# Kernel optimization log

Measured on AMD Instinct MI355X. Metric: run time of the kernel, lower is better.

The kernel has to match this reference:

```python
import jax, jax.numpy as jnp
import numpy as np

HIDDEN = 4096
HEADS = 32
HEAD_DIM = HIDDEN // HEADS  # 128; kv length must equal this (additive-bias broadcast)
B, SQ, SK = 4, 2048, HEAD_DIM


def _split_heads(x):
    # [B, T, HIDDEN] -> [B, H, T, d]
    b, t, _ = x.shape
    return x.reshape(b, t, HEADS, HEAD_DIM).transpose(0, 2, 1, 3)


def setup_inputs() -> dict:
    key = jax.random.key(0)
    ks = jax.random.split(key, 8)
    s = 1.0 / np.sqrt(HIDDEN)
    return {
        "q": jax.random.normal(ks[0], (B, SQ, HIDDEN), jnp.float32),
        "k": jax.random.normal(ks[1], (B, SK, HIDDEN), jnp.float32),
        "v": jax.random.normal(ks[2], (B, SK, HIDDEN), jnp.float32),
        "r": jax.random.normal(ks[3], (B, SQ, HIDDEN), jnp.float32),
        "Wq": jax.random.normal(ks[4], (HIDDEN, HIDDEN), jnp.float32) * s,
        "Wk": jax.random.normal(ks[5], (HIDDEN, HIDDEN), jnp.float32) * s,
        "Wv": jax.random.normal(ks[6], (HIDDEN, HIDDEN), jnp.float32) * s,
        "Wo": jax.random.normal(ks[7], (HIDDEN, HIDDEN), jnp.float32) * s,
    }


def reference(q, k, v, r, Wq, Wk, Wv, Wo):
    qh = _split_heads(q @ Wq)           # [B,H,SQ,d]
    kh = _split_heads(k @ Wk)           # [B,H,SK,d]
    vh = _split_heads(v @ Wv)           # [B,H,SK,d]
    rh = _split_heads(r @ Wo)           # [B,H,SQ,d] ; d == SK, added as bias
    scale = 1.0 / np.sqrt(HEAD_DIM).astype(np.float32)
    scores = jnp.einsum("bhqd,bhkd->bhqk", qh, kh) * scale + rh
    attn = jax.nn.softmax(scores, axis=-1)
    ctx = jnp.einsum("bhqk,bhkd->bhqd", attn, vh)       # [B,H,SQ,d]
    ctx = ctx.transpose(0, 2, 1, 3).reshape(q.shape[0], -1, HIDDEN)
    return ctx @ Wo  # Wo reused for output projection, as in source
```

## Files before the change

kernel.cpp:

```cpp
#include <hip/hip_runtime.h>
#include <hip/hip_bf16.h>

typedef unsigned short u16;
typedef unsigned int   u32;
typedef unsigned long long u64;
typedef __attribute__((ext_vector_type(8))) short short8;
typedef __attribute__((ext_vector_type(4))) float f32x4;

#define HID   4096
#define NHEAD 32
#define HD    128
#define NB    4
#define NSQ   2048
#define NSK   128
#define MROWS (NB*NSQ)
#define KROWS (NB*NSK)

__device__ __forceinline__ u16 f2bf(float f) {
  u32 u = __builtin_bit_cast(u32, f);
  u += 0x7fffu + ((u >> 16) & 1u);
  return (u16)(u >> 16);
}

__device__ __forceinline__ u64 pack4(float4 f) {
  return (u64)f2bf(f.x) | ((u64)f2bf(f.y) << 16) |
         ((u64)f2bf(f.z) << 32) | ((u64)f2bf(f.w) << 48);
}

__device__ __forceinline__ uint4 packu16x8(const u16* v) {
  uint4 o;
  o.x = (u32)v[0] | ((u32)v[1] << 16);
  o.y = (u32)v[2] | ((u32)v[3] << 16);
  o.z = (u32)v[4] | ((u32)v[5] << 16);
  o.w = (u32)v[6] | ((u32)v[7] << 16);
  return o;
}

__device__ __forceinline__ f32x4 mfma16(short8 a, short8 b, f32x4 c) {
  return __builtin_amdgcn_mfma_f32_16x16x32_bf16(a, b, c, 0, 0, 0);
}

__device__ __forceinline__ void gload_lds16(const u16* g, u16* l) {
  __builtin_amdgcn_global_load_lds((const __attribute__((address_space(1))) u32*)g,
                                   (__attribute__((address_space(3))) u32*)l, 16, 0, 0);
}

__global__ __launch_bounds__(256) void convert_bf16(const float* __restrict__ in,
                                                    u16* __restrict__ out, long long n4)
{
  long long i = (long long)blockIdx.x * blockDim.x + threadIdx.x;
  const long long stride = (long long)gridDim.x * blockDim.x;
  for (; i < n4; i += stride) {
    float4 f = ((const float4*)in)[i];
    ((u64*)out)[i] = pack4(f);
  }
}

__global__ __launch_bounds__(256) void transpose_convert(const float* __restrict__ W,
                                                         u16* __restrict__ Wt)
{
  __shared__ __align__(16) u16 tile[64][72];
  const int t = threadIdx.x;
  const int c0 = blockIdx.x * 64, r0 = blockIdx.y * 64;
  #pragma unroll
  for (int i = 0; i < 4; ++i) {
    int e = i * 1024 + t * 4;
    int rr = e >> 6, cc = e & 63;
    float4 f = *(const float4*)(W + (size_t)(r0 + rr) * HID + c0 + cc);
    *(u64*)&tile[rr][cc] = pack4(f);
  }
  __syncthreads();
  #pragma unroll
  for (int i = 0; i < 2; ++i) {
    int e = i * 2048 + t * 8;
    int cc = e >> 6, rr = e & 63;
    u16 vals[8];
    #pragma unroll
    for (int jj = 0; jj < 8; ++jj) vals[jj] = tile[rr + jj][cc];
    *(uint4*)(Wt + (size_t)(c0 + cc) * HID + r0 + rr) = packu16x8(vals);
  }
}

__global__ __launch_bounds__(256) void transpose_head(const u16* __restrict__ Vh,
                                                      u16* __restrict__ VT)
{
  __shared__ __align__(16) u16 tile[128][136];
  const int t = threadIdx.x;
  const int bh = blockIdx.x;
  const int b = bh >> 5, h = bh & 31;
  #pragma unroll
  for (int i = 0; i < 8; ++i) {
    int e = i * 2048 + t * 8;
    int tr = e >> 7, d = e & 127;
    *(uint4*)&tile[tr][d] = *(const uint4*)(Vh + ((size_t)b * NSK + tr) * HID + h * HD + d);
  }
  __syncthreads();
  #pragma unroll
  for (int i = 0; i < 8; ++i) {
    int e = i * 2048 + t * 8;
    int d = e >> 7, tt = e & 127;
    u16 vals[8];
    #pragma unroll
    for (int jj = 0; jj < 8; ++jj) vals[jj] = tile[tt + jj][d];
    *(uint4*)(VT + ((size_t)bh * HD + d) * NSK + tt) = packu16x8(vals);
  }
}


__device__ __forceinline__ short8 ldf(const u16* buf, int r, int cb) {
  return *(const short8*)(buf + r * 64 + (cb ^ ((r & 7) << 3)));
}

__device__ __forceinline__ void stage2(u16* dst, const u16* g, long off0, long off1, int tid) {
  gload_lds16(g + off0, dst + tid * 8);
  gload_lds16(g + off1, dst + 4096 + tid * 8);
}

template<bool S1, bool S2, int VM>
__device__ __forceinline__ void tile8(const u16* __restrict__ Ag, const u16* __restrict__ Bg,
                                      int kt, u16* Ac, u16* Bc, u16* Ao, u16* Bo,
                                      int wm, int wn, int g, int c16,
                                      long off0, long off1, int tid, f32x4 (&acc)[8][4])
{
  const int g8 = g * 8;
  short8 af[4][2], bf[4][2];

  #pragma unroll
  for (int i = 0; i < 4; ++i) {
    const int r = wm * 128 + i * 16 + c16;
    af[i][0] = ldf(Ac, r, g8); af[i][1] = ldf(Ac, r, 32 + g8);
  }
  #pragma unroll
  for (int j = 0; j < 2; ++j) {
    const int r = wn * 64 + j * 16 + c16;
    bf[j][0] = ldf(Bc, r, g8); bf[j][1] = ldf(Bc, r, 32 + g8);
  }
  if constexpr (S1) stage2(Ao + 8192, Ag + (size_t)128 * HID + kt + 64, off0, off1, tid);
  __builtin_amdgcn_s_barrier();
  asm volatile("s_waitcnt lgkmcnt(0)" ::: "memory");
  __builtin_amdgcn_sched_barrier(0);
  __builtin_amdgcn_s_setprio(1);
  #pragma unroll
  for (int i = 0; i < 4; ++i)
    #pragma unroll
    for (int j = 0; j < 2; ++j) {
      acc[i][j] = mfma16(af[i][0], bf[j][0], acc[i][j]);
      acc[i][j] = mfma16(af[i][1], bf[j][1], acc[i][j]);
    }
  __builtin_amdgcn_s_setprio(0);
  __builtin_amdgcn_s_barrier();

  #pragma unroll
  for (int j = 2; j < 4; ++j) {
    const int r = wn * 64 + j * 16 + c16;
    bf[j][0] = ldf(Bc, r, g8); bf[j][1] = ldf(Bc, r, 32 + g8);
  }
  if constexpr (S1) stage2(Bo + 8192, Bg + (size_t)128 * HID + kt + 64, off0, off1, tid);
  __builtin_amdgcn_s_barrier();
  asm volatile("s_waitcnt lgkmcnt(0)" ::: "memory");
  __builtin_amdgcn_sched_barrier(0);
  __builtin_amdgcn_s_setprio(1);
  #pragma unroll
  for (int i = 0; i < 4; ++i)
    #pragma unroll
    for (int j = 2; j < 4; ++j) {
      acc[i][j] = mfma16(af[i][0], bf[j][0], acc[i][j]);
      acc[i][j] = mfma16(af[i][1], bf[j][1], acc[i][j]);
    }
  __builtin_amdgcn_s_setprio(0);
  __builtin_amdgcn_s_barrier();

  #pragma unroll
  for (int i = 0; i < 4; ++i) {
    const int r = wm * 128 + 64 + i * 16 + c16;
    af[i][0] = ldf(Ac, r, g8); af[i][1] = ldf(Ac, r, 32 + g8);
  }
  if constexpr (S2) stage2(Bc, Bg + kt + 128, off0, off1, tid);
  __builtin_amdgcn_s_barrier();
  asm volatile("s_waitcnt lgkmcnt(0)" ::: "memory");
  __builtin_amdgcn_sched_barrier(0);
  __builtin_amdgcn_s_setprio(1);
  #pragma unroll
  for (int i = 0; i < 4; ++i)
    #pragma unroll
    for (int j = 0; j < 2; ++j) {
      acc[4 + i][j] = mfma16(af[i][0], bf[j][0], acc[4 + i][j]);
      acc[4 + i][j] = mfma16(af[i][1], bf[j][1], acc[4 + i][j]);
    }
  __builtin_amdgcn_s_setprio(0);
  __builtin_amdgcn_s_barrier();

  if constexpr (S2) stage2(Ac, Ag + kt + 128, off0, off1, tid);
  __builtin_amdgcn_s_barrier();
  __builtin_amdgcn_s_setprio(1);
  #pragma unroll
  for (int i = 0; i < 4; ++i)
    #pragma unroll
    for (int j = 2; j < 4; ++j) {
      acc[4 + i][j] = mfma16(af[i][0], bf[j][0], acc[4 + i][j]);
      acc[4 + i][j] = mfma16(af[i][1], bf[j][1], acc[4 + i][j]);
    }
  __builtin_amdgcn_s_setprio(0);
  if constexpr (VM == 4) {
    asm volatile("s_waitcnt vmcnt(4)" ::: "memory");
    __builtin_amdgcn_sched_barrier(0);
  } else if constexpr (VM == 0) {
    asm volatile("s_waitcnt vmcnt(0)" ::: "memory");
    __builtin_amdgcn_sched_barrier(0);
  }
  __builtin_amdgcn_s_barrier();
}

template<bool OUTF32>
__global__ __launch_bounds__(512, 2) void gemm256(const u16* __restrict__ A,
                                                  const u16* __restrict__ Bt,
                                                  void* __restrict__ Cv)
{
  __shared__ __align__(16) u16 As[2][16384];
  __shared__ __align__(16) u16 Bs[2][16384];
  const int tid = threadIdx.x;
  const int l = tid & 63, wv = tid >> 6;
  const int g = (l >> 4) & 3, c16 = l & 15;
  const int wm = wv >> 2, wn = wv & 3;

  const int ntn = gridDim.x;
  const int nwg = gridDim.x * gridDim.y;
  int wg = blockIdx.y * gridDim.x + blockIdx.x;
  wg = (wg & 7) * (nwg >> 3) + (wg >> 3);
  const int m0 = (wg / ntn) * 256, n0 = (wg % ntn) * 256;

  const u16* Ag = A + (size_t)m0 * HID;
  const u16* Bg = Bt + (size_t)n0 * HID;
  const long off0 = (long)(tid >> 3) * HID + (((tid & 7) ^ ((tid >> 3) & 7)) * 8);
  const long off1 = off0 + (long)64 * HID;

  f32x4 acc[8][4] = {};

  stage2(&Bs[0][0],    Bg,                     off0, off1, tid);
  stage2(&As[0][0],    Ag,                     off0, off1, tid);
  stage2(&As[0][8192], Ag + (size_t)128 * HID, off0, off1, tid);
  stage2(&Bs[0][8192], Bg + (size_t)128 * HID, off0, off1, tid);
  stage2(&Bs[1][0],    Bg + 64,                off0, off1, tid);
  stage2(&As[1][0],    Ag + 64,                off0, off1, tid);
  asm volatile("s_waitcnt vmcnt(4)" ::: "memory");
  __builtin_amdgcn_sched_barrier(0);
  __builtin_amdgcn_s_barrier();

  constexpr int NT = HID / 64;
  int T = 0;
  for (; T < NT - 3; T += 2) {
    tile8<true, true, 4>(Ag, Bg, T * 64,      &As[0][0], &Bs[0][0], &As[1][0], &Bs[1][0],
                         wm, wn, g, c16, off0, off1, tid, acc);
    tile8<true, true, 4>(Ag, Bg, T * 64 + 64, &As[1][0], &Bs[1][0], &As[0][0], &Bs[0][0],
                         wm, wn, g, c16, off0, off1, tid, acc);
  }
  tile8<true, false, 0>(Ag, Bg, (NT - 2) * 64, &As[0][0], &Bs[0][0], &As[1][0], &Bs[1][0],
                        wm, wn, g, c16, off0, off1, tid, acc);
  tile8<false, false, -1>(Ag, Bg, (NT - 1) * 64, &As[1][0], &Bs[1][0], &As[0][0], &Bs[0][0],
                          wm, wn, g, c16, off0, off1, tid, acc);

  #pragma unroll
  for (int mi = 0; mi < 8; ++mi)
    #pragma unroll
    for (int j = 0; j < 4; ++j)
      #pragma unroll
      for (int rr = 0; rr < 4; ++rr) {
        const size_t row = (size_t)m0 + wm * 128 + mi * 16 + g * 4 + rr;
        const size_t col = (size_t)n0 + wn * 64 + j * 16 + c16;
        if constexpr (OUTF32)
          ((float*)Cv)[row * HID + col] = acc[mi][j][rr];
        else
          ((u16*)Cv)[row * HID + col] = f2bf(acc[mi][j][rr]);
      }
}

__global__ __launch_bounds__(256) void gemm_kv(const u16* __restrict__ A,
                                               const u16* __restrict__ WkTp,
                                               const u16* __restrict__ WvTp,
                                               u16* __restrict__ Kh,
                                               u16* __restrict__ Vh)
{
  __shared__ __align__(16) u16 As_[128 * 64];
  __shared__ __align__(16) u16 Bs_[128 * 64];
  const int t = threadIdx.x;
  const int w = t >> 6, l = t & 63;
  const int g = l >> 4, c16 = l & 15;
  const int m0 = blockIdx.y * 128, n0 = blockIdx.x * 128;
  const u16* Bt = (m0 < 512) ? WkTp : WvTp;
  u16* C = (m0 < 512) ? Kh : Vh;
  const int mr0 = m0 & 511;
  const int wm = (w >> 1) * 64, wn = (w & 1) * 64;

  f32x4 acc[4][4] = {};
  for (int kt = 0; kt < HID; kt += 64) {
    #pragma unroll
    for (int i = 0; i < 4; ++i) {
      int e = i * 2048 + t * 8;
      int rr = e >> 6, cc = e & 63;
      gload_lds16(A + (size_t)(m0 + rr) * HID + kt + cc, As_ + e);
      gload_lds16(Bt + (size_t)(n0 + rr) * HID + kt + cc, Bs_ + e);
    }
    __syncthreads();
    #pragma unroll
    for (int ks = 0; ks < 2; ++ks) {
      const int ko = ks * 32 + g * 8;
      short8 af2[4], bf2[4];
      #pragma unroll
      for (int i = 0; i < 4; ++i)
        af2[i] = *(const short8*)(As_ + (wm + i * 16 + c16) * 64 + ko);
      #pragma unroll
      for (int j = 0; j < 4; ++j)
        bf2[j] = *(const short8*)(Bs_ + (wn + j * 16 + c16) * 64 + ko);
      #pragma unroll
      for (int i = 0; i < 4; ++i)
        #pragma unroll
        for (int j = 0; j < 4; ++j)
          acc[i][j] = mfma16(af2[i], bf2[j], acc[i][j]);
    }
    __syncthreads();
  }
  #pragma unroll
  for (int i = 0; i < 4; ++i)
    #pragma unroll
    for (int j = 0; j < 4; ++j)
      #pragma unroll
      for (int rr = 0; rr < 4; ++rr)
        C[(size_t)(mr0 + wm + i * 16 + g * 4 + rr) * HID + n0 + wn + j * 16 + c16] =
            f2bf(acc[i][j][rr]);
}

__global__ __launch_bounds__(256) void attn_kernel(const u16*  __restrict__ Qh,
                                                   const u16*  __restrict__ Kh,
                                                   const u16*  __restrict__ VT,
                                                   const float* __restrict__ Rh,
                                                   u16* __restrict__ ctx)
{
  __shared__ __align__(16) u16 Plds[4][32][136];
  const int t = threadIdx.x;
  const int w = t >> 6, l = t & 63;
  const int g = l >> 4, c = l & 15;
  const int qc = blockIdx.x;
  const int bh = blockIdx.y;
  const int b = bh >> 5, h = bh & 31;
  const size_t qrow0 = (size_t)b * NSQ + qc * 128 + w * 32;
  const float SCALE = 0.08838834764831845f;

  f32x4 s[2][8] = {};
  #pragma unroll
  for (int ks = 0; ks < 4; ++ks) {
    const int ko = ks * 32 + g * 8;
    short8 af[2];
    #pragma unroll
    for (int i = 0; i < 2; ++i)
      af[i] = *(const short8*)(Qh + (qrow0 + i * 16 + c) * HID + h * HD + ko);
    #pragma unroll
    for (int j = 0; j < 8; ++j) {
      short8 bfr = *(const short8*)(Kh + ((size_t)b * NSK + j * 16 + c) * HID + h * HD + ko);
      s[0][j] = mfma16(af[0], bfr, s[0][j]);
      s[1][j] = mfma16(af[1], bfr, s[1][j]);
    }
  }

  float rinv[2][4];
  #pragma unroll
  for (int i = 0; i < 2; ++i) {
    #pragma unroll
    for (int rr = 0; rr < 4; ++rr) {
      const size_t qr = qrow0 + i * 16 + g * 4 + rr;
      float vmax = -3.0e38f;
      #pragma unroll
      for (int j = 0; j < 8; ++j) {
        float bias = Rh[qr * HID + h * HD + j * 16 + c];
        float sv = s[i][j][rr] * SCALE + bias;
        s[i][j][rr] = sv;
        vmax = fmaxf(vmax, sv);
      }
      #pragma unroll
      for (int m = 1; m < 16; m <<= 1) vmax = fmaxf(vmax, __shfl_xor(vmax, m));
      float ssum = 0.f;
      #pragma unroll
      for (int j = 0; j < 8; ++j) {
        float p = __expf(s[i][j][rr] - vmax);
        s[i][j][rr] = p;
        ssum += p;
      }
      #pragma unroll
      for (int m = 1; m < 16; m <<= 1) ssum += __shfl_xor(ssum, m);
      rinv[i][rr] = 1.f / ssum;
    }
  }

  #pragma unroll
  for (int i = 0; i < 2; ++i)
    #pragma unroll
    for (int j = 0; j < 8; ++j)
      #pragma unroll
      for (int rr = 0; rr < 4; ++rr)
        Plds[w][i * 16 + g * 4 + rr][j * 16 + c] = f2bf(s[i][j][rr]);
  __syncthreads();

  #pragma unroll
  for (int i = 0; i < 2; ++i) {
    f32x4 o[8] = {};
    #pragma unroll
    for (int ks = 0; ks < 4; ++ks) {
      const int ko = ks * 32 + g * 8;
      short8 pa = *(const short8*)(&Plds[w][i * 16 + c][ko]);
      #pragma unroll
      for (int j = 0; j < 8; ++j) {
        short8 bv = *(const short8*)(VT + ((size_t)bh * HD + j * 16 + c) * NSK + ko);
        o[j] = mfma16(pa, bv, o[j]);
      }
    }
    #pragma unroll
    for (int j = 0; j < 8; ++j)
      #pragma unroll
      for (int rr = 0; rr < 4; ++rr) {
        const size_t row = qrow0 + i * 16 + g * 4 + rr;
        ctx[row * HID + h * HD + j * 16 + c] = f2bf(o[j][rr] * rinv[i][rr]);
      }
  }
}

extern "C" void kernel_launch(void* const* d_in, const int* in_sizes, int n_in,
                              void* d_out, int out_size, void* d_ws, size_t ws_size,
                              hipStream_t stream)
{
  const float* q  = (const float*)d_in[0];
  const float* k  = (const float*)d_in[1];
  const float* v  = (const float*)d_in[2];
  const float* r  = (const float*)d_in[3];
  const float* Wq = (const float*)d_in[4];
  const float* Wk = (const float*)d_in[5];
  const float* Wv = (const float*)d_in[6];
  const float* Wo = (const float*)d_in[7];
  float* out = (float*)d_out;

  char* ws = (char*)d_ws;
  #define WSMB(x) ((size_t)(x) << 20)
  u16* WoT = (u16*)(ws + WSMB(0));
  u16* Qh  = (u16*)(ws + WSMB(32));
  u16* Kh  = (u16*)(ws + WSMB(96));
  u16* Vh  = (u16*)(ws + WSMB(100));
  u16* VTb = (u16*)(ws + WSMB(104));
  u16* ctx = (u16*)(ws + WSMB(108));
  u16* kb  = (u16*)(ws + WSMB(108));
  u16* vb  = (u16*)(ws + WSMB(112));
  u16* Sb  = (u16*)(ws + WSMB(172));
  u16* WkT = (u16*)(ws + WSMB(172));
  u16* WvT = (u16*)(ws + WSMB(204));
  u16* WqT = (u16*)(ws + WSMB(236));
  const size_t needed = WSMB(268);
  if (ws_size < needed) return;

  dim3 tb(256);
  dim3 tb5(512);
  const long long nBig = (long long)MROWS * HID / 4;
  const long long nSm  = (long long)KROWS * HID / 4;

  transpose_convert<<<dim3(64, 64), tb, 0, stream>>>(Wo, WoT);

  convert_bf16<<<dim3(2048), tb, 0, stream>>>(q, Sb, nBig);
  transpose_convert<<<dim3(64, 64), tb, 0, stream>>>(Wq, WqT);
  gemm256<false><<<dim3(16, 32), tb5, 0, stream>>>(Sb, WqT, (void*)Qh);

  convert_bf16<<<dim3(2048), tb, 0, stream>>>(r, Sb, nBig);
  gemm256<true><<<dim3(16, 32), tb5, 0, stream>>>(Sb, WoT, (void*)out);

  convert_bf16<<<dim3(512), tb, 0, stream>>>(k, kb, nSm);
  convert_bf16<<<dim3(512), tb, 0, stream>>>(v, vb, nSm);
  transpose_convert<<<dim3(64, 64), tb, 0, stream>>>(Wk, WkT);
  transpose_convert<<<dim3(64, 64), tb, 0, stream>>>(Wv, WvT);
  gemm_kv<<<dim3(32, 8), tb, 0, stream>>>(kb, WkT, WvT, Kh, Vh);

  transpose_head<<<dim3(128), tb, 0, stream>>>(Vh, VTb);

  attn_kernel<<<dim3(16, 128), tb, 0, stream>>>(Qh, Kh, VTb, out, ctx);

  gemm256<true><<<dim3(16, 32), tb5, 0, stream>>>(ctx, WoT, (void*)out);
}
```

Baseline: 1.181 ms.

## Trim GEMM tile barriers and merge paired conversion launches

The bf16 GEMM inner tile now uses four workgroup barriers instead of eight. The global-to-LDS staging and the vmcnt wait are moved ahead of the last MFMA phase, so load latency overlaps with compute and waves stall less often. Separately, the Wq/Wo and Wk/Wv transpose-converts and the k/v fp32-to-bf16 conversions are each merged into one launch using an extra grid dimension, which cuts launch overhead. Removing barriers risks LDS read/write races if a wave overwrites a buffer another wave is still reading.

```diff
diff --git a/kernel.cpp b/kernel.cpp
--- a/kernel.cpp
+++ b/kernel.cpp
@@ -56,9 +56,28 @@
   }
 }
 
-__global__ __launch_bounds__(256) void transpose_convert(const float* __restrict__ W,
-                                                         u16* __restrict__ Wt)
-{
+__global__ __launch_bounds__(256) void convert_bf16_x2(const float* __restrict__ in0,
+                                                       u16* __restrict__ out0,
+                                                       const float* __restrict__ in1,
+                                                       u16* __restrict__ out1, long long n4)
+{
+  const float* in = blockIdx.y ? in1 : in0;
+  u16* out = blockIdx.y ? out1 : out0;
+  long long i = (long long)blockIdx.x * blockDim.x + threadIdx.x;
+  const long long stride = (long long)gridDim.x * blockDim.x;
+  for (; i < n4; i += stride) {
+    float4 f = ((const float4*)in)[i];
+    ((u64*)out)[i] = pack4(f);
+  }
+}
+
+__global__ __launch_bounds__(256) void transpose_convert_x2(const float* __restrict__ W0,
+                                                            u16* __restrict__ T0,
+                                                            const float* __restrict__ W1,
+                                                            u16* __restrict__ T1)
+{
+  const float* W = blockIdx.z ? W1 : W0;
+  u16* Wt = blockIdx.z ? T1 : T0;
   __shared__ __align__(16) u16 tile[64][72];
   const int t = threadIdx.x;
   const int c0 = blockIdx.x * 64, r0 = blockIdx.y * 64;
@@ -116,8 +135,8 @@
   gload_lds16(g + off1, dst + 4096 + tid * 8);
 }
 
-template<bool S1, bool S2, int VM>
-__device__ __forceinline__ void tile8(const u16* __restrict__ Ag, const u16* __restrict__ Bg,
+template<int VM, bool S1, bool S2>
+__device__ __forceinline__ void tile4(const u16* __restrict__ Ag, const u16* __restrict__ Bg,
                                       int kt, u16* Ac, u16* Bc, u16* Ao, u16* Bo,
                                       int wm, int wn, int g, int c16,
                                       long off0, long off1, int tid, f32x4 (&acc)[8][4])
@@ -148,7 +167,6 @@
       acc[i][j] = mfma16(af[i][1], bf[j][1], acc[i][j]);
     }
   __builtin_amdgcn_s_setprio(0);
-  __builtin_amdgcn_s_barrier();
 
   #pragma unroll
   for (int j = 2; j < 4; ++j) {
@@ -168,7 +186,6 @@
       acc[i][j] = mfma16(af[i][1], bf[j][1], acc[i][j]);
     }
   __builtin_amdgcn_s_setprio(0);
-  __builtin_amdgcn_s_barrier();
 
   #pragma unroll
   for (int i = 0; i < 4; ++i) {
@@ -188,10 +205,15 @@
       acc[4 + i][j] = mfma16(af[i][1], bf[j][1], acc[4 + i][j]);
     }
   __builtin_amdgcn_s_setprio(0);
+
+  if constexpr (S2) stage2(Ac, Ag + kt + 128, off0, off1, tid);
+  if constexpr (VM == 4) {
+    asm volatile("s_waitcnt vmcnt(4)" ::: "memory");
+  } else if constexpr (VM == 0) {
+    asm volatile("s_waitcnt vmcnt(0)" ::: "memory");
+  }
   __builtin_amdgcn_s_barrier();
-
-  if constexpr (S2) stage2(Ac, Ag + kt + 128, off0, off1, tid);
-  __builtin_amdgcn_s_barrier();
+  __builtin_amdgcn_sched_barrier(0);
   __builtin_amdgcn_s_setprio(1);
   #pragma unroll
   for (int i = 0; i < 4; ++i)
@@ -201,14 +223,6 @@
       acc[4 + i][j] = mfma16(af[i][1], bf[j][1], acc[4 + i][j]);
     }
   __builtin_amdgcn_s_setprio(0);
-  if constexpr (VM == 4) {
-    asm volatile("s_waitcnt vmcnt(4)" ::: "memory");
-    __builtin_amdgcn_sched_barrier(0);
-  } else if constexpr (VM == 0) {
-    asm volatile("s_waitcnt vmcnt(0)" ::: "memory");
-    __builtin_amdgcn_sched_barrier(0);
-  }
-  __builtin_amdgcn_s_barrier();
 }
 
 template<bool OUTF32>
@@ -249,14 +263,14 @@
   constexpr int NT = HID / 64;
   int T = 0;
   for (; T < NT - 3; T += 2) {
-    tile8<true, true, 4>(Ag, Bg, T * 64,      &As[0][0], &Bs[0][0], &As[1][0], &Bs[1][0],
+    tile4<4, true, true>(Ag, Bg, T * 64,      &As[0][0], &Bs[0][0], &As[1][0], &Bs[1][0],
                          wm, wn, g, c16, off0, off1, tid, acc);
-    tile8<true, true, 4>(Ag, Bg, T * 64 + 64, &As[1][0], &Bs[1][0], &As[0][0], &Bs[0][0],
+    tile4<4, true, true>(Ag, Bg, T * 64 + 64, &As[1][0], &Bs[1][0], &As[0][0], &Bs[0][0],
                          wm, wn, g, c16, off0, off1, tid, acc);
   }
-  tile8<true, false, 0>(Ag, Bg, (NT - 2) * 64, &As[0][0], &Bs[0][0], &As[1][0], &Bs[1][0],
+  tile4<0, true, false>(Ag, Bg, (NT - 2) * 64, &As[0][0], &Bs[0][0], &As[1][0], &Bs[1][0],
                         wm, wn, g, c16, off0, off1, tid, acc);
-  tile8<false, false, -1>(Ag, Bg, (NT - 1) * 64, &As[1][0], &Bs[1][0], &As[0][0], &Bs[0][0],
+  tile4<-1, false, false>(Ag, Bg, (NT - 1) * 64, &As[1][0], &Bs[1][0], &As[0][0], &Bs[0][0],
                           wm, wn, g, c16, off0, off1, tid, acc);
 
   #pragma unroll
@@ -458,19 +472,17 @@
   const long long nBig = (long long)MROWS * HID / 4;
   const long long nSm  = (long long)KROWS * HID / 4;
 
-  transpose_convert<<<dim3(64, 64), tb, 0, stream>>>(Wo, WoT);
+  transpose_convert_x2<<<dim3(64, 64, 2), tb, 0, stream>>>(Wo, WoT, Wq, WqT);
+
+  convert_bf16_x2<<<dim3(512, 2), tb, 0, stream>>>(k, kb, v, vb, nSm);
 
   convert_bf16<<<dim3(2048), tb, 0, stream>>>(q, Sb, nBig);
-  transpose_convert<<<dim3(64, 64), tb, 0, stream>>>(Wq, WqT);
   gemm256<false><<<dim3(16, 32), tb5, 0, stream>>>(Sb, WqT, (void*)Qh);
 
   convert_bf16<<<dim3(2048), tb, 0, stream>>>(r, Sb, nBig);
   gemm256<true><<<dim3(16, 32), tb5, 0, stream>>>(Sb, WoT, (void*)out);
 
-  convert_bf16<<<dim3(512), tb, 0, stream>>>(k, kb, nSm);
-  convert_bf16<<<dim3(512), tb, 0, stream>>>(v, vb, nSm);
-  transpose_convert<<<dim3(64, 64), tb, 0, stream>>>(Wk, WkT);
-  transpose_convert<<<dim3(64, 64), tb, 0, stream>>>(Wv, WvT);
+  transpose_convert_x2<<<dim3(64, 64, 2), tb, 0, stream>>>(Wk, WkT, Wv, WvT);
   gemm_kv<<<dim3(32, 8), tb, 0, stream>>>(kb, WkT, WvT, Kh, Vh);
 
   transpose_head<<<dim3(128), tb, 0, stream>>>(Vh, VTb);
```

After: 1.105 ms. 6.5% less time.
